# Kernel optimization log

Measured on AMD Instinct MI355X. Metric: run time of the kernel, lower is better.

## Reference

```python
import jax, jax.numpy as jnp
import numpy as np

N_NODES = 10000
N_EDGES = 160000
MUL = 128            # channel multiplicity
N_SPECIES = 4        # node_attrs scalars
N_RADIAL = 8         # edge_feats scalars
AVG_NEIGH = 16.0
SQRT3 = 1.7320508075688772


def setup_inputs() -> dict:
    key = jax.random.key(0)
    ks = jax.random.split(key, 16)
    inp = {}
    inp['node_attrs'] = jax.random.uniform(ks[0], (N_NODES, N_SPECIES), dtype=jnp.float32)
    inp['node_feats'] = jax.random.normal(ks[1], (N_NODES, MUL * 4), dtype=jnp.float32)  # 128x0e + 128x1o
    inp['edge_attrs'] = jax.random.normal(ks[2], (N_EDGES, 4), dtype=jnp.float32)        # 1x0e + 1x1o (SH lmax=1)
    inp['edge_feats'] = jax.random.normal(ks[3], (N_EDGES, N_RADIAL), dtype=jnp.float32)
    inp['edge_index'] = jax.random.randint(ks[4], (2, N_EDGES), 0, N_NODES, dtype=jnp.int32)
    # linear_up: per-l mixing (o3.Linear on 128x0e+128x1o)
    inp['W_up0'] = jax.random.normal(ks[5], (MUL, MUL), dtype=jnp.float32)
    inp['W_up1'] = jax.random.normal(ks[6], (MUL, MUL), dtype=jnp.float32)
    # radial MLP [8, 64, 64, 512] (conv_tp.weight_numel = 4 instructions * 128)
    inp['W_mlp1'] = jax.random.normal(ks[7], (N_RADIAL, 64), dtype=jnp.float32)
    inp['W_mlp2'] = jax.random.normal(ks[8], (64, 64), dtype=jnp.float32)
    inp['W_mlp3'] = jax.random.normal(ks[9], (64, 4 * MUL), dtype=jnp.float32)
    # linear: irreps_mid.simplify() = 256x0e + 256x1o -> 128x0e + 128x1o
    inp['W_lin0'] = jax.random.normal(ks[10], (2 * MUL, MUL), dtype=jnp.float32)
    inp['W_lin1'] = jax.random.normal(ks[11], (2 * MUL, MUL), dtype=jnp.float32)
    # skip_tp: FullyConnectedTensorProduct(target, 4x0e -> target), uvw weights per l
    inp['W_skip0'] = jax.random.normal(ks[12], (MUL, N_SPECIES, MUL), dtype=jnp.float32)
    inp['W_skip1'] = jax.random.normal(ks[13], (MUL, N_SPECIES, MUL), dtype=jnp.float32)
    inp['update_coeff_param'] = jnp.zeros((1,), dtype=jnp.float32)
    return inp


def reference(node_attrs, node_feats, edge_attrs, edge_feats, edge_index,
              W_up0, W_up1, W_mlp1, W_mlp2, W_mlp3, W_lin0, W_lin1,
              W_skip0, W_skip1, update_coeff_param):
    N = node_feats.shape[0]
    # split node feats into irrep blocks: scalars [N,128], vectors [N,128,3]
    s = node_feats[:, :MUL]
    v = node_feats[:, MUL:].reshape(N, MUL, 3)
    # linear_up (o3.Linear, fan-in normalized)
    inv_up = 1.0 / jnp.sqrt(jnp.float32(MUL))
    s = (s @ W_up0) * inv_up
    v = jnp.einsum('nui,uw->nwi', v, W_up1) * inv_up
    # radial MLP -> per-edge TP weights (e3nn FullyConnectedNet style, fan-in normalized, silu)
    h = jax.nn.silu((edge_feats @ W_mlp1) / jnp.sqrt(jnp.float32(N_RADIAL)))
    h = jax.nn.silu((h @ W_mlp2) / jnp.sqrt(jnp.float32(64)))
    tpw = (h @ W_mlp3) / jnp.sqrt(jnp.float32(64))  # [E, 512]
    # instruction order (sorted by output irrep): 0e*0e->0e, 1o*1o->0e, 0e*1o->1o, 1o*0e->1o
    w_a, w_b, w_c, w_d = tpw[:, :MUL], tpw[:, MUL:2*MUL], tpw[:, 2*MUL:3*MUL], tpw[:, 3*MUL:]
    sender, receiver = edge_index[0], edge_index[1]
    xs = s[sender]          # [E,128] gather
    xv = v[sender]          # [E,128,3]
    ea_s = edge_attrs[:, :1]    # [E,1]
    ea_v = edge_attrs[:, 1:4]   # [E,3]
    # CG tensor-product messages ('uvu', component norm)
    m0 = w_a * xs * ea_s                                        # 0e x 0e -> 0e
    m1 = w_b * (jnp.einsum('eui,ei->eu', xv, ea_v) / SQRT3)      # 1o x 1o -> 0e
    m2 = (w_c * xs)[:, :, None] * ea_v[:, None, :]               # 0e x 1o -> 1o
    m3 = w_d[:, :, None] * xv * ea_s[:, :, None]                 # 1o x 0e -> 1o
    ms = jnp.concatenate([m0, m1], axis=1)                       # [E,256]
    mv = jnp.concatenate([m2, m3], axis=1)                       # [E,256,3]
    # scatter-sum to receiver nodes
    Ms = jax.ops.segment_sum(ms, receiver, num_segments=N)       # [N,256]
    Mv = jax.ops.segment_sum(mv, receiver, num_segments=N)       # [N,256,3]
    # linear (256x0e+256x1o -> 128x0e+128x1o), divided by avg_num_neighbors
    inv_lin = 1.0 / (jnp.sqrt(jnp.float32(2 * MUL)) * AVG_NEIGH)
    S = (Ms @ W_lin0) * inv_lin                                  # [N,128]
    V = jnp.einsum('nui,uw->nwi', Mv, W_lin1) * inv_lin          # [N,128,3]
    # skip_tp: FullyConnectedTensorProduct(message, node_attrs) with uvw weights
    inv_sk = 1.0 / jnp.sqrt(jnp.float32(MUL * N_SPECIES))
    sc_s = jnp.einsum('nu,nv,uvw->nw', S, node_attrs, W_skip0) * inv_sk
    sc_v = jnp.einsum('nui,nv,uvw->nwi', V, node_attrs, W_skip1) * inv_sk
    # residual stream mixing (sc=False branch)
    c = jax.nn.sigmoid(update_coeff_param)                       # [1]
    c_old = jax.lax.rsqrt(c * c + 1.0)
    c_new = c * c_old
    S = c_old * S + c_new * sc_s
    V = c_old * V + c_new * sc_v
    # reshape_irreps: [N, mul, 1 + 3]
    out = jnp.concatenate([S[:, :, None], V], axis=-1)           # [N,128,4]
    return out
```

## Files before the change

kernel.cpp:

```cpp
#include <hip/hip_runtime.h>

#define MUL 128

typedef __attribute__((ext_vector_type(8))) short bf16x8;
typedef __attribute__((ext_vector_type(4))) short bf16x4;
typedef __attribute__((ext_vector_type(4))) float f32x4;

__device__ __constant__ float kINV_UP   = 0.08838834764831845f;
__device__ __constant__ float kINV_L1   = 0.35355339059327373f;
__device__ __constant__ float kINV_L2   = 0.125f;
__device__ __constant__ float kINV_L3   = 0.125f;
__device__ __constant__ float kINV_LIN  = 0.00390625f;
__device__ __constant__ float kINV_SK   = 0.044194173824159216f;
__device__ __constant__ float kINV_SQ3  = 0.5773502691896258f;

#define WAVE_LDS_SYNC() asm volatile("s_waitcnt lgkmcnt(0)" ::: "memory")

static __device__ __forceinline__ short f2bf(float f) {
  unsigned u = __float_as_uint(f);
  unsigned r = (u + 0x7FFFu + ((u >> 16) & 1u)) >> 16;
  return (short)r;
}

__global__ __launch_bounds__(256) void k_cvtcnt(
    const float* __restrict__ W_up0, const float* __restrict__ W_up1,
    const float* __restrict__ W_lin0, const float* __restrict__ W_lin1,
    const float* __restrict__ W_sk0, const float* __restrict__ W_sk1,
    const float* __restrict__ W_mlp2, const float* __restrict__ W_mlp3,
    short* __restrict__ W0T, short* __restrict__ W1T,
    short* __restrict__ Wl0T, short* __restrict__ Wl1T,
    short* __restrict__ Wsk0T, short* __restrict__ Wsk1T,
    short* __restrict__ W2T, short* __restrict__ W3T,
    const int* __restrict__ eidx, int* __restrict__ cnt, int E, int CVT_B) {
  int blk = blockIdx.x;
  if (blk >= CVT_B) {
    int e = (blk - CVT_B) * 256 + threadIdx.x;
    if (e < E) atomicAdd(&cnt[eidx[E + e]], 1);
    return;
  }
  int id = blk * 256 + threadIdx.x;
  if (id < 16384) {
    int w = id >> 7, u = id & 127;
    W0T[id] = f2bf(W_up0[u * 128 + w]);
    return;
  }
  id -= 16384;
  if (id < 16384) {
    int w = id >> 7, u = id & 127;
    W1T[id] = f2bf(W_up1[u * 128 + w]);
    return;
  }
  id -= 16384;
  if (id < 32768) {
    int w = id >> 8, u = id & 255;
    Wl0T[id] = f2bf(W_lin0[u * 128 + w]);
    return;
  }
  id -= 32768;
  if (id < 32768) {
    int w = id >> 8, u = id & 255;
    Wl1T[id] = f2bf(W_lin1[u * 128 + w]);
    return;
  }
  id -= 32768;
  if (id < 65536) {
    int w = id >> 9, k = id & 511;
    int v = k >> 7, u = k & 127;
    Wsk0T[id] = f2bf(W_sk0[(u * 4 + v) * 128 + w]);
    return;
  }
  id -= 65536;
  if (id < 65536) {
    int w = id >> 9, k = id & 511;
    int v = k >> 7, u = k & 127;
    Wsk1T[id] = f2bf(W_sk1[(u * 4 + v) * 128 + w]);
    return;
  }
  id -= 65536;
  if (id < 4096) {
    int c = id >> 6, k = id & 63;
    W2T[id] = f2bf(W_mlp2[k * 64 + c]);
    return;
  }
  id -= 4096;
  if (id < 32768) {
    int c = id >> 6, k = id & 63;
    W3T[id] = f2bf(W_mlp3[k * 512 + c]);
  }
}

__global__ __launch_bounds__(1024) void k_scan(const int* __restrict__ cnt,
                                               int* __restrict__ offs,
                                               int* __restrict__ cursor, int N) {
  __shared__ int part[1024];
  const int t = threadIdx.x;
  int CH = (N + 1023) >> 10;
  if (CH > 16) CH = 16;
  const int base = t * CH;
  int loc[16];
  int s = 0;
  for (int i = 0; i < CH; ++i) {
    int idx = base + i;
    loc[i] = (idx < N) ? cnt[idx] : 0;
    s += loc[i];
  }
  part[t] = s;
  __syncthreads();
  for (int off = 1; off < 1024; off <<= 1) {
    int v = part[t];
    int add = (t >= off) ? part[t - off] : 0;
    __syncthreads();
    part[t] = v + add;
    __syncthreads();
  }
  int excl = part[t] - s;
  for (int i = 0; i < CH; ++i) {
    int idx = base + i;
    if (idx < N) { offs[idx] = excl; cursor[idx] = excl; }
    excl += loc[i];
  }
  if (t == 1023) offs[N] = part[1023];
}

__global__ __launch_bounds__(256) void k_fused3(
    const int* __restrict__ eidx, int* __restrict__ cursor, uint2* __restrict__ recs,
    const float* __restrict__ nf, const short* __restrict__ W0T,
    const short* __restrict__ W1T, float* __restrict__ s_up, float* __restrict__ v_up,
    const float* __restrict__ ef, const float* __restrict__ W1f,
    const short* __restrict__ W2T, const short* __restrict__ W3T,
    unsigned* __restrict__ tpw2, int N, int E, int MLP_B, int UP_B) {
  __shared__ __align__(16) char smem[48128];
  const int t = threadIdx.x;
  int blk = blockIdx.x;

  if (blk < MLP_B) {
    float* sW1  = (float*)smem;
    short* sW2T = (short*)(smem + 2048);
    short* sh1  = (short*)(smem + 11264);
    short* sh2  = (short*)(smem + 29696);

    for (int i = t * 4; i < 512; i += 1024)
      *reinterpret_cast<float4*>(&sW1[i]) = *reinterpret_cast<const float4*>(W1f + i);
    for (int i = t * 8; i < 4096; i += 2048) {
      int r = i >> 6, c = i & 63;
      *reinterpret_cast<bf16x8*>(&sW2T[r * 72 + c]) =
          *reinterpret_cast<const bf16x8*>(&W2T[r * 64 + c]);
    }
    __syncthreads();

    const int w = t >> 6, l = t & 63, li = l & 15, g = l >> 4;
    const int eb = blk * 128 + w * 32;
    const int es0 = eb + li, es1 = eb + 16 + li;
    short* h1r0 = sh1 + (w * 32 + li) * 72;
    short* h1r1 = sh1 + (w * 32 + 16 + li) * 72;
    short* h2r0 = sh2 + (w * 32 + li) * 72;
    short* h2r1 = sh2 + (w * 32 + 16 + li) * 72;

    {
#pragma unroll
      for (int s = 0; s < 2; ++s) {
        const int e = s ? es1 : es0;
        short* h1row = s ? h1r1 : h1r0;
        float4 qa = {0.f, 0.f, 0.f, 0.f}, qb = {0.f, 0.f, 0.f, 0.f};
        if (e < E) {
          qa = *reinterpret_cast<const float4*>(ef + (size_t)e * 8);
          qb = *reinterpret_cast<const float4*>(ef + (size_t)e * 8 + 4);
        }
        const float x[8] = {qa.x, qa.y, qa.z, qa.w, qb.x, qb.y, qb.z, qb.w};
        bf16x8 p0, p1;
#pragma unroll
        for (int j = 0; j < 16; ++j) {
          int col = g * 16 + j;
          float a = 0.f;
#pragma unroll
          for (int k = 0; k < 8; ++k) a += x[k] * sW1[k * 64 + col];
          a *= kINV_L1;
          short hv = f2bf(a / (1.f + __expf(-a)));
          if (j < 8) p0[j] = hv; else p1[j - 8] = hv;
        }
        *reinterpret_cast<bf16x8*>(&h1row[g * 16])     = p0;
        *reinterpret_cast<bf16x8*>(&h1row[g * 16 + 8]) = p1;
      }
    }
    WAVE_LDS_SYNC();

    {
      bf16x8 hb0[2], hb1[2];
      hb0[0] = *reinterpret_cast<const bf16x8*>(&h1r0[g * 8]);
      hb1[0] = *reinterpret_cast<const bf16x8*>(&h1r0[32 + g * 8]);
      hb0[1] = *reinterpret_cast<const bf16x8*>(&h1r1[g * 8]);
      hb1[1] = *reinterpret_cast<const bf16x8*>(&h1r1[32 + g * 8]);
#pragma unroll
      for (int ct = 0; ct < 4; ++ct) {
        const short* wrow = &sW2T[(ct * 16 + li) * 72];
        bf16x8 a0 = *reinterpret_cast<const bf16x8*>(&wrow[g * 8]);
        bf16x8 a1 = *reinterpret_cast<const bf16x8*>(&wrow[32 + g * 8]);
#pragma unroll
        for (int s = 0; s < 2; ++s) {
          f32x4 acc = {0.f, 0.f, 0.f, 0.f};
          acc = __builtin_amdgcn_mfma_f32_16x16x32_bf16(a0, hb0[s], acc, 0, 0, 0);
          acc = __builtin_amdgcn_mfma_f32_16x16x32_bf16(a1, hb1[s], acc, 0, 0, 0);
          bf16x4 hq;
#pragma unroll
          for (int r = 0; r < 4; ++r) {
            float a = acc[r] * kINV_L2;
            hq[r] = f2bf(a / (1.f + __expf(-a)));
          }
          *reinterpret_cast<bf16x4*>(&((s ? h2r1 : h2r0)[ct * 16 + g * 4])) = hq;
        }
      }
    }
    WAVE_LDS_SYNC();

    {
      bf16x8 b0[2], b1[2];
      b0[0] = *reinterpret_cast<const bf16x8*>(&h2r0[g * 8]);
      b1[0] = *reinterpret_cast<const bf16x8*>(&h2r0[32 + g * 8]);
      b0[1] = *reinterpret_cast<const bf16x8*>(&h2r1[g * 8]);
      b1[1] = *reinterpret_cast<const bf16x8*>(&h2r1[32 + g * 8]);
      const bool ok0 = es0 < E, ok1 = es1 < E;

      bf16x8 c0, c1, c2, c3;
      {
        const int rowA = li;
        c0 = *reinterpret_cast<const bf16x8*>(&W3T[(size_t)rowA * 64 + g * 8]);
        c1 = *reinterpret_cast<const bf16x8*>(&W3T[(size_t)rowA * 64 + 32 + g * 8]);
        c2 = *reinterpret_cast<const bf16x8*>(&W3T[(size_t)(rowA + 256) * 64 + g * 8]);
        c3 = *reinterpret_cast<const bf16x8*>(&W3T[(size_t)(rowA + 256) * 64 + 32 + g * 8]);
      }
#pragma unroll
      for (int rt = 0; rt < 16; ++rt) {
        bf16x8 n0, n1, n2, n3;
        const bool pf = (rt < 15);
        if (pf) {
          const int rowA = (rt + 1) * 16 + li;
          n0 = *reinterpret_cast<const bf16x8*>(&W3T[(size_t)rowA * 64 + g * 8]);
          n1 = *reinterpret_cast<const bf16x8*>(&W3T[(size_t)rowA * 64 + 32 + g * 8]);
          n2 = *reinterpret_cast<const bf16x8*>(&W3T[(size_t)(rowA + 256) * 64 + g * 8]);
          n3 = *reinterpret_cast<const bf16x8*>(&W3T[(size_t)(rowA + 256) * 64 + 32 + g * 8]);
        }
#pragma unroll
        for (int s = 0; s < 2; ++s) {
          f32x4 accA = {0.f, 0.f, 0.f, 0.f};
          f32x4 accB = {0.f, 0.f, 0.f, 0.f};
          accA = __builtin_amdgcn_mfma_f32_16x16x32_bf16(c0, b0[s], accA, 0, 0, 0);
          accA = __builtin_amdgcn_mfma_f32_16x16x32_bf16(c1, b1[s], accA, 0, 0, 0);
          accB = __builtin_amdgcn_mfma_f32_16x16x32_bf16(c2, b0[s], accB, 0, 0, 0);
          accB = __builtin_amdgcn_mfma_f32_16x16x32_bf16(c3, b1[s], accB, 0, 0, 0);
          if (s ? ok1 : ok0) {
            uint4 d;
            unsigned* dp = &d.x;
#pragma unroll
            for (int r = 0; r < 4; ++r) {
              unsigned lo = (unsigned)(unsigned short)f2bf(accA[r] * kINV_L3);
              unsigned hi = (unsigned)(unsigned short)f2bf(accB[r] * kINV_L3);
              dp[r] = lo | (hi << 16);
            }
            *reinterpret_cast<uint4*>(
                &tpw2[(size_t)(s ? es1 : es0) * 256 + rt * 16 + g * 4]) = d;
          }
        }
        if (pf) { c0 = n0; c1 = n1; c2 = n2; c3 = n3; }
      }
    }
    return;
  }
  blk -= MLP_B;

  if (blk < UP_B) {
    short* lsA = (short*)smem;
    const int nb = blk * 16;

    for (int base = t * 8; base < 16 * 512; base += 256 * 8) {
      int n = base >> 9, j0 = base & 511;
      float vals[8];
      if (nb + n < N) {
        float4 q0 = *reinterpret_cast<const float4*>(nf + (size_t)(nb + n) * 512 + j0);
        float4 q1 = *reinterpret_cast<const float4*>(nf + (size_t)(nb + n) * 512 + j0 + 4);
        vals[0] = q0.x; vals[1] = q0.y; vals[2] = q0.z; vals[3] = q0.w;
        vals[4] = q1.x; vals[5] = q1.y; vals[6] = q1.z; vals[7] = q1.w;
      } else {
#pragma unroll
        for (int e = 0; e < 8; ++e) vals[e] = 0.f;
      }
#pragma unroll
      for (int e = 0; e < 8; ++e) {
        int idx = j0 + e;
        if (idx < 128) {
          lsA[(0 * 16 + n) * 136 + idx] = f2bf(vals[e]);
        } else {
          unsigned q = idx - 128;
          unsigned u = q / 3u;
          unsigned i = q - u * 3u;
          lsA[((1 + i) * 16 + n) * 136 + u] = f2bf(vals[e]);
        }
      }
    }
    __syncthreads();

    const int c = t >> 6;
    const int lane = t & 63;
    const int col = lane & 15;
    const int g = lane >> 4;

    const short* WT = c ? W1T : W0T;

    bf16x8 af[4];
#pragma unroll
    for (int kk = 0; kk < 4; ++kk)
      af[kk] = *reinterpret_cast<const bf16x8*>(&lsA[(c * 16 + col) * 136 + kk * 32 + g * 8]);

#pragma unroll
    for (int nt = 0; nt < 8; ++nt) {
      f32x4 acc = {0.f, 0.f, 0.f, 0.f};
#pragma unroll
      for (int kk = 0; kk < 4; ++kk) {
        bf16x8 bf = *reinterpret_cast<const bf16x8*>(&WT[(size_t)(nt * 16 + col) * 128 + kk * 32 + g * 8]);
        acc = __builtin_amdgcn_mfma_f32_16x16x32_bf16(af[kk], bf, acc, 0, 0, 0);
      }
#pragma unroll
      for (int r = 0; r < 4; ++r) {
        int nd = nb + g * 4 + r;
        if (nd < N) {
          float val = acc[r] * kINV_UP;
          if (c == 0) s_up[(size_t)nd * 128 + nt * 16 + col] = val;
          else        v_up[(size_t)nd * 384 + (c - 1) * 128 + nt * 16 + col] = val;
        }
      }
    }
    return;
  }
  blk -= UP_B;

  int e = blk * 256 + t;
  if (e < E) {
    int r = eidx[E + e];
    int snd = eidx[e];
    int p = atomicAdd(&cursor[r], 1);
    recs[p] = make_uint2((unsigned)e, (unsigned)snd);
  }
}

__global__ __launch_bounds__(256) void k_gather(
    const uint2* __restrict__ recs, const int* __restrict__ offs,
    const unsigned* __restrict__ tpw2, const float* __restrict__ eattr,
    const float* __restrict__ s_up, const float* __restrict__ v_up,
    float* __restrict__ Ms, float* __restrict__ Mv, int N) {
  const int t = threadIdx.x;
  const int n = blockIdx.x * 4 + (t >> 6);
  if (n >= N) return;
  const int l = t & 63;
  const int u0 = l * 2;

  float aMsS0 = 0.f, aMsS1 = 0.f;
  float aMsV0 = 0.f, aMsV1 = 0.f;
  float aVs[3][2] = {};
  float aVv[3][2] = {};

  const int e0 = offs[n], e1 = offs[n + 1];

  for (int p0 = e0; p0 < e1; p0 += 4) {
    const int last = e1 - 1;
    uint2 rc0 = recs[p0];
    uint2 rc1 = recs[min(p0 + 1, last)];
    uint2 rc2 = recs[min(p0 + 2, last)];
    uint2 rc3 = recs[min(p0 + 3, last)];

    float4 ea0 = *reinterpret_cast<const float4*>(eattr + (size_t)rc0.x * 4);
    float4 ea1 = *reinterpret_cast<const float4*>(eattr + (size_t)rc1.x * 4);
    float4 ea2 = *reinterpret_cast<const float4*>(eattr + (size_t)rc2.x * 4);
    float4 ea3 = *reinterpret_cast<const float4*>(eattr + (size_t)rc3.x * 4);
    uint2 qs0 = *reinterpret_cast<const uint2*>(tpw2 + (size_t)rc0.x * 256 + u0);
    uint2 qs1 = *reinterpret_cast<const uint2*>(tpw2 + (size_t)rc1.x * 256 + u0);
    uint2 qs2 = *reinterpret_cast<const uint2*>(tpw2 + (size_t)rc2.x * 256 + u0);
    uint2 qs3 = *reinterpret_cast<const uint2*>(tpw2 + (size_t)rc3.x * 256 + u0);
    uint2 qv0 = *reinterpret_cast<const uint2*>(tpw2 + (size_t)rc0.x * 256 + 128 + u0);
    uint2 qv1 = *reinterpret_cast<const uint2*>(tpw2 + (size_t)rc1.x * 256 + 128 + u0);
    uint2 qv2 = *reinterpret_cast<const uint2*>(tpw2 + (size_t)rc2.x * 256 + 128 + u0);
    uint2 qv3 = *reinterpret_cast<const uint2*>(tpw2 + (size_t)rc3.x * 256 + 128 + u0);
    float2 xs0 = *reinterpret_cast<const float2*>(s_up + (size_t)rc0.y * 128 + u0);
    float2 xs1 = *reinterpret_cast<const float2*>(s_up + (size_t)rc1.y * 128 + u0);
    float2 xs2 = *reinterpret_cast<const float2*>(s_up + (size_t)rc2.y * 128 + u0);
    float2 xs3 = *reinterpret_cast<const float2*>(s_up + (size_t)rc3.y * 128 + u0);
    const float* xvp0 = v_up + (size_t)rc0.y * 384 + u0;
    const float* xvp1 = v_up + (size_t)rc1.y * 384 + u0;
    const float* xvp2 = v_up + (size_t)rc2.y * 384 + u0;
    const float* xvp3 = v_up + (size_t)rc3.y * 384 + u0;
    float2 xa0 = *reinterpret_cast<const float2*>(xvp0);
    float2 xb0 = *reinterpret_cast<const float2*>(xvp0 + 128);
    float2 xc0 = *reinterpret_cast<const float2*>(xvp0 + 256);
    float2 xa1 = *reinterpret_cast<const float2*>(xvp1);
    float2 xb1 = *reinterpret_cast<const float2*>(xvp1 + 128);
    float2 xc1 = *reinterpret_cast<const float2*>(xvp1 + 256);
    float2 xa2 = *reinterpret_cast<const float2*>(xvp2);
    float2 xb2 = *reinterpret_cast<const float2*>(xvp2 + 128);
    float2 xc2 = *reinterpret_cast<const float2*>(xvp2 + 256);
    float2 xa3 = *reinterpret_cast<const float2*>(xvp3);
    float2 xb3 = *reinterpret_cast<const float2*>(xvp3 + 128);
    float2 xc3 = *reinterpret_cast<const float2*>(xvp3 + 256);

    const int m = e1 - p0;
    if (m < 4) {
      float k1 = (m > 1) ? 1.f : 0.f;
      float k2 = (m > 2) ? 1.f : 0.f;
      ea1.x *= k1; ea1.y *= k1; ea1.z *= k1; ea1.w *= k1;
      ea2.x *= k2; ea2.y *= k2; ea2.z *= k2; ea2.w *= k2;
      ea3.x = 0.f; ea3.y = 0.f; ea3.z = 0.f; ea3.w = 0.f;
    }

#define ACC_EDGE(EA, QS, QV, XS, XA, XB, XC)                                   \
    {                                                                          \
      float tA0 = __uint_as_float(QS.x << 16);                                 \
      float tB0 = __uint_as_float(QS.x & 0xFFFF0000u);                         \
      float tA1 = __uint_as_float(QS.y << 16);                                 \
      float tB1 = __uint_as_float(QS.y & 0xFFFF0000u);                         \
      aMsS0 += tA0 * XS.x * EA.x;                                              \
      aMsS1 += tA1 * XS.y * EA.x;                                              \
      float wc0 = tB0 * XS.x, wc1 = tB1 * XS.y;                                \
      aVs[0][0] += wc0 * EA.y; aVs[0][1] += wc1 * EA.y;                        \
      aVs[1][0] += wc0 * EA.z; aVs[1][1] += wc1 * EA.z;                        \
      aVs[2][0] += wc0 * EA.w; aVs[2][1] += wc1 * EA.w;                        \
      float uA0 = __uint_as_float(QV.x << 16);                                 \
      float uB0 = __uint_as_float(QV.x & 0xFFFF0000u);                         \
      float uA1 = __uint_as_float(QV.y << 16);                                 \
      float uB1 = __uint_as_float(QV.y & 0xFFFF0000u);                         \
      float dot0 = XA.x * EA.y + XB.x * EA.z + XC.x * EA.w;                    \
      float dot1 = XA.y * EA.y + XB.y * EA.z + XC.y * EA.w;                    \
      aMsV0 += uA0 * dot0 * kINV_SQ3;                                          \
      aMsV1 += uA1 * dot1 * kINV_SQ3;                                          \
      float wd0 = uB0 * EA.x, wd1 = uB1 * EA.x;                                \
      aVv[0][0] += wd0 * XA.x; aVv[0][1] += wd1 * XA.y;                        \
      aVv[1][0] += wd0 * XB.x; aVv[1][1] += wd1 * XB.y;                        \
      aVv[2][0] += wd0 * XC.x; aVv[2][1] += wd1 * XC.y;                        \
    }

    ACC_EDGE(ea0, qs0, qv0, xs0, xa0, xb0, xc0)
    ACC_EDGE(ea1, qs1, qv1, xs1, xa1, xb1, xc1)
    ACC_EDGE(ea2, qs2, qv2, xs2, xa2, xb2, xc2)
    ACC_EDGE(ea3, qs3, qv3, xs3, xa3, xb3, xc3)
#undef ACC_EDGE
  }

  *reinterpret_cast<float2*>(Ms + (size_t)n * 256 + u0)       = make_float2(aMsS0, aMsS1);
  *reinterpret_cast<float2*>(Ms + (size_t)n * 256 + 128 + u0) = make_float2(aMsV0, aMsV1);
#pragma unroll
  for (int i = 0; i < 3; ++i) {
    *reinterpret_cast<float2*>(Mv + (size_t)n * 768 + i * 256 + u0) =
        make_float2(aVs[i][0], aVs[i][1]);
    *reinterpret_cast<float2*>(Mv + (size_t)n * 768 + i * 256 + 128 + u0) =
        make_float2(aVv[i][0], aVv[i][1]);
  }
}

__global__ __launch_bounds__(256) void k_linskip(
    const float* __restrict__ Ms, const float* __restrict__ Mv,
    const short* __restrict__ Wl0T, const short* __restrict__ Wl1T,
    const short* __restrict__ Wsk0T, const short* __restrict__ Wsk1T,
    const float* __restrict__ attrs, const float* __restrict__ upd,
    float* __restrict__ out, int N) {
  __shared__ __align__(16) short lsA[4][16][264];
  __shared__ __align__(16) short lsS[4][16][136];
  __shared__ float sat[16][4];
  const int nb = blockIdx.x * 16;
  const int t = threadIdx.x;

  for (int base = t * 4; base < 16 * 1024; base += 1024) {
    int n = base >> 10, j = base & 1023;
    int comp = j >> 8, u = j & 255;
    float4 q = {0.f, 0.f, 0.f, 0.f};
    if (nb + n < N) {
      const float* src = (comp == 0) ? (Ms + (size_t)(nb + n) * 256 + u)
                                     : (Mv + (size_t)(nb + n) * 768 + (size_t)(comp - 1) * 256 + u);
      q = *reinterpret_cast<const float4*>(src);
    }
    lsA[comp][n][u + 0] = f2bf(q.x);
    lsA[comp][n][u + 1] = f2bf(q.y);
    lsA[comp][n][u + 2] = f2bf(q.z);
    lsA[comp][n][u + 3] = f2bf(q.w);
  }
  if (t < 64) {
    int n = t >> 2, v = t & 3;
    sat[n][v] = (nb + n < N) ? attrs[(size_t)(nb + n) * 4 + v] : 0.f;
  }
  __syncthreads();

  const int c = t >> 6;
  const int lane = t & 63;
  const int col = lane & 15;
  const int g = lane >> 4;

  const short* WLT = c ? Wl1T : Wl0T;
  const short* WST = c ? Wsk1T : Wsk0T;

  bf16x8 af1[8];
#pragma unroll
  for (int kk = 0; kk < 8; ++kk)
    af1[kk] = *reinterpret_cast<const bf16x8*>(&lsA[c][col][kk * 32 + g * 8]);

  f32x4 Sreg[8];
#pragma unroll
  for (int nt = 0; nt < 8; ++nt) {
    f32x4 acc = {0.f, 0.f, 0.f, 0.f};
#pragma unroll
    for (int kk = 0; kk < 8; ++kk) {
      bf16x8 bf = *reinterpret_cast<const bf16x8*>(&WLT[(size_t)(nt * 16 + col) * 256 + kk * 32 + g * 8]);
      acc = __builtin_amdgcn_mfma_f32_16x16x32_bf16(af1[kk], bf, acc, 0, 0, 0);
    }
#pragma unroll
    for (int r = 0; r < 4; ++r) acc[r] *= kINV_LIN;
    Sreg[nt] = acc;
#pragma unroll
    for (int r = 0; r < 4; ++r)
      lsS[c][g * 4 + r][nt * 16 + col] = f2bf(acc[r]);
  }

  float satr[4][4];
#pragma unroll
  for (int r = 0; r < 4; ++r)
#pragma unroll
    for (int v = 0; v < 4; ++v) satr[r][v] = sat[g * 4 + r][v];

  __syncthreads();

  bf16x8 af2[4];
#pragma unroll
  for (int kk = 0; kk < 4; ++kk)
    af2[kk] = *reinterpret_cast<const bf16x8*>(&lsS[c][col][kk * 32 + g * 8]);

  const float p = upd[0];
  const float cc = 1.f / (1.f + __expf(-p));
  const float c_old = rsqrtf(cc * cc + 1.f);
  const float c_new = cc * c_old;

#pragma unroll
  for (int nt = 0; nt < 8; ++nt) {
    float fin[4] = {0.f, 0.f, 0.f, 0.f};
#pragma unroll
    for (int v = 0; v < 4; ++v) {
      f32x4 tmp = {0.f, 0.f, 0.f, 0.f};
#pragma unroll
      for (int kk = 0; kk < 4; ++kk) {
        bf16x8 bf = *reinterpret_cast<const bf16x8*>(&WST[(size_t)(nt * 16 + col) * 512 + v * 128 + kk * 32 + g * 8]);
        tmp = __builtin_amdgcn_mfma_f32_16x16x32_bf16(af2[kk], bf, tmp, 0, 0, 0);
      }
#pragma unroll
      for (int r = 0; r < 4; ++r) fin[r] += satr[r][v] * tmp[r];
    }
#pragma unroll
    for (int r = 0; r < 4; ++r) {
      int nd = nb + g * 4 + r;
      if (nd < N) {
        float val = c_old * Sreg[nt][r] + c_new * fin[r] * kINV_SK;
        out[((size_t)nd * 128 + nt * 16 + col) * 4 + c] = val;
      }
    }
  }
}

extern "C" void kernel_launch(void* const* d_in, const int* in_sizes, int n_in,
                              void* d_out, int out_size, void* d_ws, size_t ws_size,
                              hipStream_t stream) {
  const float* node_attrs = (const float*)d_in[0];
  const float* node_feats = (const float*)d_in[1];
  const float* edge_attrs = (const float*)d_in[2];
  const float* edge_feats = (const float*)d_in[3];
  const int*   edge_index = (const int*)d_in[4];
  const float* W_up0  = (const float*)d_in[5];
  const float* W_up1  = (const float*)d_in[6];
  const float* W_mlp1 = (const float*)d_in[7];
  const float* W_mlp2 = (const float*)d_in[8];
  const float* W_mlp3 = (const float*)d_in[9];
  const float* W_lin0 = (const float*)d_in[10];
  const float* W_lin1 = (const float*)d_in[11];
  const float* W_skip0 = (const float*)d_in[12];
  const float* W_skip1 = (const float*)d_in[13];
  const float* upd = (const float*)d_in[14];
  float* out = (float*)d_out;

  const int N = in_sizes[0] / 4;
  const int E = in_sizes[4] / 2;

  float* ws = (float*)d_ws;
  float* s_up = ws;
  float* v_up = s_up + (size_t)N * 128;
  float* Ms   = v_up + (size_t)N * 384;
  float* Mv   = Ms + (size_t)N * 256;
  int* cnt    = (int*)(Mv + (size_t)N * 768);
  int* offs   = cnt + N;
  int* cursor = offs + N + 1;
  uint2* recs = (uint2*)((((uintptr_t)(cursor + N)) + 7) & ~(uintptr_t)7);

  short* wbase = (short*)((((uintptr_t)(recs + E)) + 15) & ~(uintptr_t)15);
  short* W0T   = wbase;
  short* W1T   = W0T + 16384;
  short* Wl0T  = W1T + 16384;
  short* Wl1T  = Wl0T + 32768;
  short* Wsk0T = Wl1T + 32768;
  short* Wsk1T = Wsk0T + 65536;
  short* W2T   = Wsk1T + 65536;
  short* W3T   = W2T + 4096;
  unsigned* tpw2 = (unsigned*)(W3T + 32768);

  const int CVT_B = (266240 + 255) / 256;
  const int CNT_B = (E + 255) / 256;
  const int MLP_B = (E + 127) / 128;
  const int UP_B  = (N + 15) / 16;
  const int SC_B  = (E + 255) / 256;

  hipMemsetAsync(cnt, 0, (size_t)N * sizeof(int), stream);

  k_cvtcnt<<<CVT_B + CNT_B, 256, 0, stream>>>(
      W_up0, W_up1, W_lin0, W_lin1, W_skip0, W_skip1, W_mlp2, W_mlp3,
      W0T, W1T, Wl0T, Wl1T, Wsk0T, Wsk1T, W2T, W3T,
      edge_index, cnt, E, CVT_B);
  k_scan<<<1, 1024, 0, stream>>>(cnt, offs, cursor, N);
  k_fused3<<<MLP_B + UP_B + SC_B, 256, 0, stream>>>(
      edge_index, cursor, recs,
      node_feats, W0T, W1T, s_up, v_up,
      edge_feats, W_mlp1, W2T, W3T, tpw2, N, E, MLP_B, UP_B);
  k_gather<<<(N + 3) / 4, 256, 0, stream>>>(recs, offs, tpw2, edge_attrs,
                                            s_up, v_up, Ms, Mv, N);
  k_linskip<<<(N + 15) / 16, 256, 0, stream>>>(Ms, Mv, Wl0T, Wl1T, Wsk0T, Wsk1T,
                                               node_attrs, upd, out, N);
}
```

Baseline: 269.8 us.

## Store radial MLP weights in receiver-sorted order for contiguous gather reads

New measurement: 277.1 us. 1.03x slower.

```diff
diff --git a/kernel.cpp b/kernel.cpp
--- a/kernel.cpp
+++ b/kernel.cpp
@@ -122,13 +122,25 @@
   if (t == 1023) offs[N] = part[1023];
 }
 
-__global__ __launch_bounds__(256) void k_fused3(
-    const int* __restrict__ eidx, int* __restrict__ cursor, uint2* __restrict__ recs,
+__global__ __launch_bounds__(256) void k_scatter(
+    const int* __restrict__ eidx, int* __restrict__ cursor,
+    uint2* __restrict__ recs, int E) {
+  int e = blockIdx.x * 256 + threadIdx.x;
+  if (e < E) {
+    int r = eidx[E + e];
+    int snd = eidx[e];
+    int p = atomicAdd(&cursor[r], 1);
+    recs[p] = make_uint2((unsigned)e, (unsigned)snd);
+  }
+}
+
+__global__ __launch_bounds__(256) void k_mlpup(
+    const uint2* __restrict__ recs,
     const float* __restrict__ nf, const short* __restrict__ W0T,
     const short* __restrict__ W1T, float* __restrict__ s_up, float* __restrict__ v_up,
     const float* __restrict__ ef, const float* __restrict__ W1f,
     const short* __restrict__ W2T, const short* __restrict__ W3T,
-    unsigned* __restrict__ tpw2, int N, int E, int MLP_B, int UP_B) {
+    unsigned* __restrict__ tpw2, int N, int E, int MLP_B) {
   __shared__ __align__(16) char smem[48128];
   const int t = threadIdx.x;
   int blk = blockIdx.x;
@@ -149,8 +161,11 @@
     __syncthreads();
 
     const int w = t >> 6, l = t & 63, li = l & 15, g = l >> 4;
-    const int eb = blk * 128 + w * 32;
-    const int es0 = eb + li, es1 = eb + 16 + li;
+    const int pb = blk * 128 + w * 32;
+    const int ps0 = pb + li, ps1 = pb + 16 + li;
+    const bool ok0 = ps0 < E, ok1 = ps1 < E;
+    const int eid0 = ok0 ? (int)recs[ps0].x : 0;
+    const int eid1 = ok1 ? (int)recs[ps1].x : 0;
     short* h1r0 = sh1 + (w * 32 + li) * 72;
     short* h1r1 = sh1 + (w * 32 + 16 + li) * 72;
     short* h2r0 = sh2 + (w * 32 + li) * 72;
@@ -159,12 +174,13 @@
     {
 #pragma unroll
       for (int s = 0; s < 2; ++s) {
-        const int e = s ? es1 : es0;
+        const bool ok = s ? ok1 : ok0;
+        const int eid = s ? eid1 : eid0;
         short* h1row = s ? h1r1 : h1r0;
         float4 qa = {0.f, 0.f, 0.f, 0.f}, qb = {0.f, 0.f, 0.f, 0.f};
-        if (e < E) {
-          qa = *reinterpret_cast<const float4*>(ef + (size_t)e * 8);
-          qb = *reinterpret_cast<const float4*>(ef + (size_t)e * 8 + 4);
+        if (ok) {
+          qa = *reinterpret_cast<const float4*>(ef + (size_t)eid * 8);
+          qb = *reinterpret_cast<const float4*>(ef + (size_t)eid * 8 + 4);
         }
         const float x[8] = {qa.x, qa.y, qa.z, qa.w, qb.x, qb.y, qb.z, qb.w};
         bf16x8 p0, p1;
@@ -218,7 +234,6 @@
       b1[0] = *reinterpret_cast<const bf16x8*>(&h2r0[32 + g * 8]);
       b0[1] = *reinterpret_cast<const bf16x8*>(&h2r1[g * 8]);
       b1[1] = *reinterpret_cast<const bf16x8*>(&h2r1[32 + g * 8]);
-      const bool ok0 = es0 < E, ok1 = es1 < E;
 
       bf16x8 c0, c1, c2, c3;
       {
@@ -257,7 +272,7 @@
               dp[r] = lo | (hi << 16);
             }
             *reinterpret_cast<uint4*>(
-                &tpw2[(size_t)(s ? es1 : es0) * 256 + rt * 16 + g * 4]) = d;
+                &tpw2[(size_t)(s ? ps1 : ps0) * 256 + rt * 16 + g * 4]) = d;
           }
         }
         if (pf) { c0 = n0; c1 = n1; c2 = n2; c3 = n3; }
@@ -267,7 +282,7 @@
   }
   blk -= MLP_B;
 
-  if (blk < UP_B) {
+  {
     short* lsA = (short*)smem;
     const int nb = blk * 16;
 
@@ -328,16 +343,6 @@
         }
       }
     }
-    return;
-  }
-  blk -= UP_B;
-
-  int e = blk * 256 + t;
-  if (e < E) {
-    int r = eidx[E + e];
-    int snd = eidx[e];
-    int p = atomicAdd(&cursor[r], 1);
-    recs[p] = make_uint2((unsigned)e, (unsigned)snd);
   }
 }
 
@@ -358,26 +363,29 @@
   float aVv[3][2] = {};
 
   const int e0 = offs[n], e1 = offs[n + 1];
+  const int last = e1 - 1;
 
   for (int p0 = e0; p0 < e1; p0 += 4) {
-    const int last = e1 - 1;
+    const int p1 = min(p0 + 1, last);
+    const int p2 = min(p0 + 2, last);
+    const int p3 = min(p0 + 3, last);
     uint2 rc0 = recs[p0];
-    uint2 rc1 = recs[min(p0 + 1, last)];
-    uint2 rc2 = recs[min(p0 + 2, last)];
-    uint2 rc3 = recs[min(p0 + 3, last)];
+    uint2 rc1 = recs[p1];
+    uint2 rc2 = recs[p2];
+    uint2 rc3 = recs[p3];
 
     float4 ea0 = *reinterpret_cast<const float4*>(eattr + (size_t)rc0.x * 4);
     float4 ea1 = *reinterpret_cast<const float4*>(eattr + (size_t)rc1.x * 4);
     float4 ea2 = *reinterpret_cast<const float4*>(eattr + (size_t)rc2.x * 4);
     float4 ea3 = *reinterpret_cast<const float4*>(eattr + (size_t)rc3.x * 4);
-    uint2 qs0 = *reinterpret_cast<const uint2*>(tpw2 + (size_t)rc0.x * 256 + u0);
-    uint2 qs1 = *reinterpret_cast<const uint2*>(tpw2 + (size_t)rc1.x * 256 + u0);
-    uint2 qs2 = *reinterpret_cast<const uint2*>(tpw2 + (size_t)rc2.x * 256 + u0);
-    uint2 qs3 = *reinterpret_cast<const uint2*>(tpw2 + (size_t)rc3.x * 256 + u0);
-    uint2 qv0 = *reinterpret_cast<const uint2*>(tpw2 + (size_t)rc0.x * 256 + 128 + u0);
-    uint2 qv1 = *reinterpret_cast<const uint2*>(tpw2 + (size_t)rc1.x * 256 + 128 + u0);
-    uint2 qv2 = *reinterpret_cast<const uint2*>(tpw2 + (size_t)rc2.x * 256 + 128 + u0);
-    uint2 qv3 = *reinterpret_cast<const uint2*>(tpw2 + (size_t)rc3.x * 256 + 128 + u0);
+    uint2 qs0 = *reinterpret_cast<const uint2*>(tpw2 + (size_t)p0 * 256 + u0);
+    uint2 qs1 = *reinterpret_cast<const uint2*>(tpw2 + (size_t)p1 * 256 + u0);
+    uint2 qs2 = *reinterpret_cast<const uint2*>(tpw2 + (size_t)p2 * 256 + u0);
+    uint2 qs3 = *reinterpret_cast<const uint2*>(tpw2 + (size_t)p3 * 256 + u0);
+    uint2 qv0 = *reinterpret_cast<const uint2*>(tpw2 + (size_t)p0 * 256 + 128 + u0);
+    uint2 qv1 = *reinterpret_cast<const uint2*>(tpw2 + (size_t)p1 * 256 + 128 + u0);
+    uint2 qv2 = *reinterpret_cast<const uint2*>(tpw2 + (size_t)p2 * 256 + 128 + u0);
+    uint2 qv3 = *reinterpret_cast<const uint2*>(tpw2 + (size_t)p3 * 256 + 128 + u0);
     float2 xs0 = *reinterpret_cast<const float2*>(s_up + (size_t)rc0.y * 128 + u0);
     float2 xs1 = *reinterpret_cast<const float2*>(s_up + (size_t)rc1.y * 128 + u0);
     float2 xs2 = *reinterpret_cast<const float2*>(s_up + (size_t)rc2.y * 128 + u0);
@@ -603,9 +611,9 @@
 
   const int CVT_B = (266240 + 255) / 256;
   const int CNT_B = (E + 255) / 256;
+  const int SC_B  = (E + 255) / 256;
   const int MLP_B = (E + 127) / 128;
   const int UP_B  = (N + 15) / 16;
-  const int SC_B  = (E + 255) / 256;
 
   hipMemsetAsync(cnt, 0, (size_t)N * sizeof(int), stream);
 
@@ -614,10 +622,10 @@
       W0T, W1T, Wl0T, Wl1T, Wsk0T, Wsk1T, W2T, W3T,
       edge_index, cnt, E, CVT_B);
   k_scan<<<1, 1024, 0, stream>>>(cnt, offs, cursor, N);
-  k_fused3<<<MLP_B + UP_B + SC_B, 256, 0, stream>>>(
-      edge_index, cursor, recs,
-      node_feats, W0T, W1T, s_up, v_up,
-      edge_feats, W_mlp1, W2T, W3T, tpw2, N, E, MLP_B, UP_B);
+  k_scatter<<<SC_B, 256, 0, stream>>>(edge_index, cursor, recs, E);
+  k_mlpup<<<MLP_B + UP_B, 256, 0, stream>>>(
+      recs, node_feats, W0T, W1T, s_up, v_up,
+      edge_feats, W_mlp1, W2T, W3T, tpw2, N, E, MLP_B);
   k_gather<<<(N + 3) / 4, 256, 0, stream>>>(recs, offs, tpw2, edge_attrs,
                                             s_up, v_up, Ms, Mv, N);
   k_linskip<<<(N + 15) / 16, 256, 0, stream>>>(Ms, Mv, Wl0T, Wl1T, Wsk0T, Wsk1T,
```
